# Kernel optimization log

Hardware: AMD Instinct MI355X
Metric: run time of the kernel (lower is better)

The kernel has to match this reference:

```python
import jax, jax.numpy as jnp
import numpy as np
from itertools import combinations
from math import comb

CONV_RANGE = 5
CORR_ORDER = 5
K = (2 * CONV_RANGE + 1) ** 2 // 2        # 60 active filter positions
FH, FW = CONV_RANGE + 1, 2 * CONV_RANGE + 1
B, H, W = 1, 4, 4


def build_filters():
    # One binary filter per k-subset (k=1..5) of the 60 positions; order[f] = |subset|.
    perms = sum(comb(K, i) for i in range(1, CORR_ORDER + 1))  # 5_985_197
    filters = np.zeros((perms, FH * FW), dtype=np.float32)
    order = np.zeros(perms, dtype=np.float32)
    row = 0
    for i in range(1, CORR_ORDER + 1):
        c = np.array(list(combinations(range(K), i)), dtype=np.int64)  # [C(K,i), i]
        rows = np.arange(row, row + c.shape[0])
        filters[rows[:, None], c] = 1.0
        order[rows] = float(i)
        row += c.shape[0]
    return filters, order


def setup_inputs() -> dict:
    key = jax.random.key(0)
    k1, k2, k3, k4 = jax.random.split(key, 4)
    filters_np, order_np = build_filters()
    perms = filters_np.shape[0]
    x = jax.random.randint(k1, (B, 1, H, W), 0, 2).astype(jnp.int32)
    # torch zero-inits correlation.weight; we use small random weights for a non-trivial baseline
    w_corr = jax.random.normal(k2, (1, perms), dtype=jnp.float32) * 0.02
    den_w = jax.random.normal(k3, (1, 1), dtype=jnp.float32)
    den_b = jax.random.normal(k4, (1,), dtype=jnp.float32)
    return {"x": x, "filters": jnp.asarray(filters_np),
            "order_index": jnp.asarray(order_np),
            "w_corr": w_corr, "den_w": den_w, "den_b": den_b}


def reference(x, filters, order_index, w_corr, den_w, den_b):
    b, _, h, w = x.shape
    xb = (x == 1).astype(jnp.float32)[:, 0]  # [B,H,W] binary occupancy
    xp = jnp.pad(xb, ((0, 0), (CONV_RANGE, CONV_RANGE), (CONV_RANGE, CONV_RANGE)))
    # patches[b,y,x, dy*FW+dx] = xp[b, y+dy, x+dx]; equals F.conv2d(pad=5) output cropped to first H rows
    patches = jnp.stack([xp[:, dy:dy + h, dx:dx + w]
                         for dy in range(FH) for dx in range(FW)], axis=-1)  # [B,H,W,66]
    counts = jnp.einsum('bhwk,pk->bhwp', patches, filters)  # [B,H,W,perms]
    # order-i filter "fires" iff all i selected sites are occupied (count == i)
    ind = (counts == order_index).astype(jnp.float32)
    y = jnp.einsum('bhwp,p->bhw', ind, w_corr[0])
    y = y + den_b[0] + den_w[0, 0] * 0.0  # den_corr(torch.zeros(1)) = bias
    out = jnp.stack([jnp.full_like(y, -100.0), -y, y], axis=1)  # [B,3,H,W]
    return out
```

## Files before the change

kernel.cpp:

```cpp
#include <hip/hip_runtime.h>

#define OFF2 60
#define OFF3 1830
#define OFF4 36050
#define OFF5 523685

__global__ __launch_bounds__(256) void brutesolver_kernel(
        const int* __restrict__ x,
        const float* __restrict__ w,
        const float* __restrict__ den_b,
        float* __restrict__ out) {
    __shared__ int   P[5][61];
    __shared__ int   CB[16][6];
    __shared__ int   s_occ[16];
    __shared__ int   s_m;
    __shared__ int   scnt[256];
    __shared__ int   sbuf[4944];
    __shared__ float sred[256];

    const int tid = threadIdx.x;
    const int pix = blockIdx.x;
    const int py = pix >> 2, px = pix & 3;

    if (tid < 64) {
        bool flag = false;
        if (tid < 60) {
            int iy = py + tid / 11 - 5;
            int ix = px + tid % 11 - 5;
            flag = (iy >= 0) && (iy < 4) && (ix >= 0) && (ix < 4) && (x[iy * 4 + ix] == 1);
        }
        unsigned long long mask = __ballot(flag);
        if (flag) s_occ[__popcll(mask & ((1ull << tid) - 1))] = tid;
        if (tid == 0) s_m = (int)__popcll(mask);
    }
    if (tid <= 60) {
        long long n = 60 - tid;
        P[0][tid] = tid;
        P[1][tid] = 1770    - (int)(n * (n - 1) / 2);
        P[2][tid] = 34220   - (int)(n * (n - 1) * (n - 2) / 6);
        P[3][tid] = 487635  - (int)(n * (n - 1) * (n - 2) * (n - 3) / 24);
        P[4][tid] = 5461512 - (int)(n * (n - 1) * (n - 2) * (n - 3) * (n - 4) / 120);
    }
    if (tid < 16) {
        long long n = tid;
        CB[tid][0] = 1;
        CB[tid][1] = tid;
        CB[tid][2] = (int)(n * (n - 1) / 2);
        CB[tid][3] = (int)(n * (n - 1) * (n - 2) / 6);
        CB[tid][4] = (int)(n * (n - 1) * (n - 2) * (n - 3) / 24);
        CB[tid][5] = (int)(n * (n - 1) * (n - 2) * (n - 3) * (n - 4) / 120);
    }
    __syncthreads();

    const int m = s_m;
    const int nPairs = CB[m][2];
    const int nTrip  = CB[m][3];

    int pA = -1, pB = -1;
    if (tid < nPairs) {
        int q = tid, a = 0;
        while (CB[m - 1 - a][1] <= q) { q -= CB[m - 1 - a][1]; ++a; }
        pA = a; pB = a + 1 + q;
    }
    int tA0 = -1, tB0 = 0, tC0 = 0, tA1 = -1, tB1 = 0, tC1 = 0;
    int cnt = (tid < m ? 1 : 0) + (pA >= 0 ? 1 : 0);
    if (tid < nTrip) {
        int q = tid, a = 0;
        while (CB[m - 1 - a][2] <= q) { q -= CB[m - 1 - a][2]; ++a; }
        int b = a + 1;
        while (CB[m - 1 - b][1] <= q) { q -= CB[m - 1 - b][1]; ++b; }
        tA0 = a; tB0 = b; tC0 = b + 1 + q;
        int t = m - 1 - tC0;
        cnt += 1 + t + t * (t - 1) / 2;
    }
    if (tid + 256 < nTrip) {
        int q = tid + 256, a = 0;
        while (CB[m - 1 - a][2] <= q) { q -= CB[m - 1 - a][2]; ++a; }
        int b = a + 1;
        while (CB[m - 1 - b][1] <= q) { q -= CB[m - 1 - b][1]; ++b; }
        tA1 = a; tB1 = b; tC1 = b + 1 + q;
        int t = m - 1 - tC1;
        cnt += 1 + t + t * (t - 1) / 2;
    }

    scnt[tid] = cnt;
    __syncthreads();
    for (int off = 1; off < 256; off <<= 1) {
        int v = (tid >= off) ? scnt[tid - off] : 0;
        __syncthreads();
        scnt[tid] += v;
        __syncthreads();
    }
    int pos = scnt[tid] - cnt;
    const int T = scnt[255];

    if (tid < m) sbuf[pos++] = s_occ[tid];
    if (pA >= 0) {
        int c0 = s_occ[pA], c1 = s_occ[pB];
        sbuf[pos++] = OFF2 + P[1][c0] + (c1 - c0 - 1);
    }
    auto emitTriple = [&](int ia, int ib, int ic) {
        int c0 = s_occ[ia], c1 = s_occ[ib], c2 = s_occ[ic];
        sbuf[pos++] = OFF3 + P[2][c0] + P[1][c1] - P[1][c0 + 1] + (c2 - c1 - 1);
        int b4 = P[3][c0] + P[2][c1] - P[2][c0 + 1] + P[1][c2] - P[1][c1 + 1];
        int b5 = P[4][c0] + P[3][c1] - P[3][c0 + 1] + P[2][c2] - P[2][c1 + 1];
        for (int di = ic + 1; di < m; ++di) {
            int c3 = s_occ[di];
            sbuf[pos++] = OFF4 + b4 + (c3 - c2 - 1);
            int b5d = b5 + P[1][c3] - P[1][c2 + 1];
            for (int ei = di + 1; ei < m; ++ei) {
                int c4 = s_occ[ei];
                sbuf[pos++] = OFF5 + b5d + (c4 - c3 - 1);
            }
        }
    };
    if (tA0 >= 0) emitTriple(tA0, tB0, tC0);
    if (tA1 >= 0) emitTriple(tA1, tB1, tC1);
    __syncthreads();

    float a0 = 0.f, a1 = 0.f, a2 = 0.f, a3 = 0.f;
    int g = tid;
    for (; g + 768 < T; g += 1024) {
        a0 += w[sbuf[g]];
        a1 += w[sbuf[g + 256]];
        a2 += w[sbuf[g + 512]];
        a3 += w[sbuf[g + 768]];
    }
    for (; g < T; g += 256) a0 += w[sbuf[g]];
    float acc = (a0 + a1) + (a2 + a3);

    sred[tid] = acc;
    __syncthreads();
    for (int s = 128; s > 0; s >>= 1) {
        if (tid < s) sred[tid] += sred[tid + s];
        __syncthreads();
    }
    if (tid == 0) {
        float y = sred[0] + den_b[0];
        out[pix]      = -100.0f;
        out[16 + pix] = -y;
        out[32 + pix] = y;
    }
}

extern "C" void kernel_launch(void* const* d_in, const int* in_sizes, int n_in,
                              void* d_out, int out_size, void* d_ws, size_t ws_size,
                              hipStream_t stream) {
    const int*   x     = (const int*)d_in[0];
    const float* w     = (const float*)d_in[3];
    const float* den_b = (const float*)d_in[5];
    float* out = (float*)d_out;
    brutesolver_kernel<<<16, 256, 0, stream>>>(x, w, den_b, out);
}
```

Before: 12.95 us.

## Replace prefix-scan offsets with closed-form positions and use wave-shuffle reduction

Removes the block-wide Hillis-Steele prefix scan over per-thread emit counts (16 barriers) by computing each triple's output position in closed form from binomial tables. The final sum switches from a shared-memory tree with 8 barriers to a 64-lane shuffle reduction plus a 4-entry shared combine. The gather loop is fully unrolled to 20 independent loads so all weight fetches can be in flight together. This adds register pressure and depends on the closed-form offset being correct.

```diff
diff --git a/kernel.cpp b/kernel.cpp
--- a/kernel.cpp
+++ b/kernel.cpp
@@ -14,9 +14,8 @@
     __shared__ int   CB[16][6];
     __shared__ int   s_occ[16];
     __shared__ int   s_m;
-    __shared__ int   scnt[256];
     __shared__ int   sbuf[4944];
-    __shared__ float sred[256];
+    __shared__ float swave[4];
 
     const int tid = threadIdx.x;
     const int pix = blockIdx.x;
@@ -55,88 +54,69 @@
     const int m = s_m;
     const int nPairs = CB[m][2];
     const int nTrip  = CB[m][3];
+    const int T = m + nPairs + nTrip + CB[m][4] + CB[m][5];
 
-    int pA = -1, pB = -1;
+    if (tid < m) sbuf[tid] = s_occ[tid];
+
     if (tid < nPairs) {
         int q = tid, a = 0;
         while (CB[m - 1 - a][1] <= q) { q -= CB[m - 1 - a][1]; ++a; }
-        pA = a; pB = a + 1 + q;
-    }
-    int tA0 = -1, tB0 = 0, tC0 = 0, tA1 = -1, tB1 = 0, tC1 = 0;
-    int cnt = (tid < m ? 1 : 0) + (pA >= 0 ? 1 : 0);
-    if (tid < nTrip) {
-        int q = tid, a = 0;
-        while (CB[m - 1 - a][2] <= q) { q -= CB[m - 1 - a][2]; ++a; }
-        int b = a + 1;
-        while (CB[m - 1 - b][1] <= q) { q -= CB[m - 1 - b][1]; ++b; }
-        tA0 = a; tB0 = b; tC0 = b + 1 + q;
-        int t = m - 1 - tC0;
-        cnt += 1 + t + t * (t - 1) / 2;
-    }
-    if (tid + 256 < nTrip) {
-        int q = tid + 256, a = 0;
-        while (CB[m - 1 - a][2] <= q) { q -= CB[m - 1 - a][2]; ++a; }
-        int b = a + 1;
-        while (CB[m - 1 - b][1] <= q) { q -= CB[m - 1 - b][1]; ++b; }
-        tA1 = a; tB1 = b; tC1 = b + 1 + q;
-        int t = m - 1 - tC1;
-        cnt += 1 + t + t * (t - 1) / 2;
+        int b = a + 1 + q;
+        int c0 = s_occ[a], c1 = s_occ[b];
+        sbuf[m + tid] = OFF2 + P[1][c0] + (c1 - c0 - 1);
     }
 
-    scnt[tid] = cnt;
-    __syncthreads();
-    for (int off = 1; off < 256; off <<= 1) {
-        int v = (tid >= off) ? scnt[tid - off] : 0;
-        __syncthreads();
-        scnt[tid] += v;
-        __syncthreads();
-    }
-    int pos = scnt[tid] - cnt;
-    const int T = scnt[255];
+    #pragma unroll
+    for (int rep = 0; rep < 2; ++rep) {
+        int j = tid + rep * 256;
+        if (j < nTrip) {
+            int q = j, a = 0;
+            while (CB[m - 1 - a][2] <= q) { q -= CB[m - 1 - a][2]; ++a; }
+            int b = a + 1;
+            while (CB[m - 1 - b][1] <= q) { q -= CB[m - 1 - b][1]; ++b; }
+            int c = b + 1 + q;
+            int A1 = (CB[m][3] - CB[m - a][3]) + (CB[m][4] - CB[m - a][4])
+                   + (CB[m][5] - CB[m - a][5]);
+            int A2 = (CB[m - 1 - a][2] - CB[m - b][2]) + (CB[m - 1 - a][3] - CB[m - b][3])
+                   + (CB[m - 1 - a][4] - CB[m - b][4]);
+            int A3 = (CB[m - 1 - b][1] - CB[m - c][1]) + (CB[m - 1 - b][2] - CB[m - c][2])
+                   + (CB[m - 1 - b][3] - CB[m - c][3]);
+            int pos = m + nPairs + A1 + A2 + A3;
 
-    if (tid < m) sbuf[pos++] = s_occ[tid];
-    if (pA >= 0) {
-        int c0 = s_occ[pA], c1 = s_occ[pB];
-        sbuf[pos++] = OFF2 + P[1][c0] + (c1 - c0 - 1);
-    }
-    auto emitTriple = [&](int ia, int ib, int ic) {
-        int c0 = s_occ[ia], c1 = s_occ[ib], c2 = s_occ[ic];
-        sbuf[pos++] = OFF3 + P[2][c0] + P[1][c1] - P[1][c0 + 1] + (c2 - c1 - 1);
-        int b4 = P[3][c0] + P[2][c1] - P[2][c0 + 1] + P[1][c2] - P[1][c1 + 1];
-        int b5 = P[4][c0] + P[3][c1] - P[3][c0 + 1] + P[2][c2] - P[2][c1 + 1];
-        for (int di = ic + 1; di < m; ++di) {
-            int c3 = s_occ[di];
-            sbuf[pos++] = OFF4 + b4 + (c3 - c2 - 1);
-            int b5d = b5 + P[1][c3] - P[1][c2 + 1];
-            for (int ei = di + 1; ei < m; ++ei) {
-                int c4 = s_occ[ei];
-                sbuf[pos++] = OFF5 + b5d + (c4 - c3 - 1);
+            int c0 = s_occ[a], c1 = s_occ[b], c2 = s_occ[c];
+            sbuf[pos++] = OFF3 + P[2][c0] + P[1][c1] - P[1][c0 + 1] + (c2 - c1 - 1);
+            int b4 = P[3][c0] + P[2][c1] - P[2][c0 + 1] + P[1][c2] - P[1][c1 + 1];
+            int b5 = P[4][c0] + P[3][c1] - P[3][c0 + 1] + P[2][c2] - P[2][c1 + 1];
+            for (int di = c + 1; di < m; ++di) {
+                int c3 = s_occ[di];
+                sbuf[pos++] = OFF4 + b4 + (c3 - c2 - 1);
+                int b5d = b5 + P[1][c3] - P[1][c2 + 1];
+                for (int ei = di + 1; ei < m; ++ei) {
+                    int c4 = s_occ[ei];
+                    sbuf[pos++] = OFF5 + b5d + (c4 - c3 - 1);
+                }
             }
         }
-    };
-    if (tA0 >= 0) emitTriple(tA0, tB0, tC0);
-    if (tA1 >= 0) emitTriple(tA1, tB1, tC1);
+    }
     __syncthreads();
 
-    float a0 = 0.f, a1 = 0.f, a2 = 0.f, a3 = 0.f;
-    int g = tid;
-    for (; g + 768 < T; g += 1024) {
-        a0 += w[sbuf[g]];
-        a1 += w[sbuf[g + 256]];
-        a2 += w[sbuf[g + 512]];
-        a3 += w[sbuf[g + 768]];
+    float av[20];
+    #pragma unroll
+    for (int u = 0; u < 20; ++u) {
+        av[u] = 0.f;
+        int g = tid + 256 * u;
+        if (g < T) av[u] = w[sbuf[g]];
     }
-    for (; g < T; g += 256) a0 += w[sbuf[g]];
-    float acc = (a0 + a1) + (a2 + a3);
+    float acc = 0.f;
+    #pragma unroll
+    for (int u = 0; u < 20; ++u) acc += av[u];
 
-    sred[tid] = acc;
+    #pragma unroll
+    for (int off = 32; off > 0; off >>= 1) acc += __shfl_xor(acc, off);
+    if ((tid & 63) == 0) swave[tid >> 6] = acc;
     __syncthreads();
-    for (int s = 128; s > 0; s >>= 1) {
-        if (tid < s) sred[tid] += sred[tid + s];
-        __syncthreads();
-    }
     if (tid == 0) {
-        float y = sred[0] + den_b[0];
+        float y = swave[0] + swave[1] + swave[2] + swave[3] + den_b[0];
         out[pix]      = -100.0f;
         out[16 + pix] = -y;
         out[32 + pix] = y;
```

Measured after the change: 15.53 us. 1.2x slower.
